# Performance work log

Hardware: AMD Instinct MI355X
Metric: run time of the kernel (lower is better)

The kernel has to match this reference:

```python
import jax, jax.numpy as jnp
import numpy as np

N = 51200      # total nodes
G = 128        # graphs
E = 614400     # edges
IN, HID, OUT = 128, 64, 64


def gcn_conv(x, W, b, src, dst, n):
    # PyG GCNConv: add self loops, symmetric normalization, aggregate src->dst
    h = x @ W                                   # [n, d_out]
    loop = jnp.arange(n)
    s = jnp.concatenate([src, loop])
    d = jnp.concatenate([dst, loop])
    deg = jax.ops.segment_sum(jnp.ones_like(d, dtype=h.dtype), d, num_segments=n)
    dinv = jnp.where(deg > 0, jax.lax.rsqrt(deg), 0.0)
    norm = dinv[s] * dinv[d]                    # [E+n]
    out = jax.ops.segment_sum(h[s] * norm[:, None], d, num_segments=n)
    return out + b


def setup_inputs() -> dict:
    key = jax.random.key(0)
    ks = jax.random.split(key, 8)
    x = jax.random.normal(ks[0], (N, IN), dtype=jnp.float32)
    edge_index = jax.random.randint(ks[1], (2, E), 0, N, dtype=jnp.int64)
    batch = jnp.repeat(jnp.arange(G, dtype=jnp.int64), N // G)   # 400 nodes/graph
    rootindex = jnp.arange(G, dtype=jnp.int64) * (N // G)
    root = jax.random.normal(ks[2], (G, IN), dtype=jnp.float32)
    W1 = jax.random.normal(ks[3], (IN, HID), dtype=jnp.float32) / np.sqrt(IN)
    b1 = jnp.zeros((HID,), dtype=jnp.float32)
    W2 = jax.random.normal(ks[4], (HID + IN, OUT), dtype=jnp.float32) / np.sqrt(HID + IN)
    b2 = jnp.zeros((OUT,), dtype=jnp.float32)
    return {"x": x, "edge_index": edge_index, "batch": batch,
            "rootindex": rootindex, "root": root,
            "W1": W1, "b1": b1, "W2": W2, "b2": b2}


def reference(x, edge_index, batch, rootindex, root, W1, b1, W2, b2):
    n = x.shape[0]
    g = root.shape[0]
    src, dst = edge_index[0], edge_index[1]

    h1 = gcn_conv(x, W1, b1, src, dst, n)        # conv1 output (= x2 in torch)
    root_extend1 = root[batch]                   # broadcast root feats to nodes
    h = jax.nn.relu(jnp.concatenate([h1, root_extend1], axis=1))
    # F.dropout(training=False) -> identity (eval mode)
    h2 = jax.nn.relu(gcn_conv(h, W2, b2, src, dst, n))
    root_extend2 = h1[rootindex][batch]          # x2[rootindex[batch_id]] per node
    out = jnp.concatenate([h2, root_extend2], axis=1)   # [N, OUT+HID]
    # scatter_mean over graphs
    counts = jax.ops.segment_sum(jnp.ones((n,), dtype=out.dtype), batch, num_segments=g)
    pooled = jax.ops.segment_sum(out, batch, num_segments=g) / counts[:, None]
    return pooled                                 # [G, OUT+HID]
```

## Files before the change

### kernel.cpp

```cpp
#include <hip/hip_runtime.h>
#include <hip/hip_bf16.h>
#include <math.h>

#define DIN 128
#define DH  64
#define CAPP 32
#define BKSH 8
#define BKN  256
#define BCAP 4096
#define BCSH 12
#define ACH  4096

typedef short  short8 __attribute__((ext_vector_type(8)));
typedef float  f32x4  __attribute__((ext_vector_type(4)));
typedef unsigned short us4 __attribute__((ext_vector_type(4)));

__device__ __forceinline__ short f2bf(float v) {
    return __builtin_bit_cast(short, __float2bfloat16(v));
}
__device__ __forceinline__ float bf2f(unsigned short v) {
    return __builtin_bit_cast(float, ((unsigned)v) << 16);
}


__device__ __forceinline__ void wpack_body(const float* __restrict__ W, short8* __restrict__ o, int fid) {
    int l  = fid & 63, f = fid >> 6;
    int kc = f >> 2, nt = f & 3;
    int kb = kc * 32 + (l >> 4) * 8;
    int c  = nt * 16 + (l & 15);
    short8 r;
    #pragma unroll
    for (int j = 0; j < 8; ++j) r[j] = f2bf(W[(size_t)(kb + j) * DH + c]);
    o[fid] = r;
}

template<int KDIM>
__device__ __forceinline__ void mgemm_body(int wid, int lane, const float* __restrict__ feat,
                                           const short8* __restrict__ wpk,
                                           unsigned short* __restrict__ out, int N) {
    constexpr int KCH = KDIM / 32;
    int ntiles = (N + 15) >> 4;
    if (wid >= ntiles) return;

    short8 bf[KCH][4];
    #pragma unroll
    for (int kc = 0; kc < KCH; ++kc)
        #pragma unroll
        for (int nt = 0; nt < 4; ++nt)
            bf[kc][nt] = wpk[(kc * 4 + nt) * 64 + lane];

    f32x4 acc[4] = {};

    int arow = wid * 16 + (lane & 15);
    if (arow >= N) arow = N - 1;

    #pragma unroll
    for (int kc = 0; kc < KCH; ++kc) {
        const float* ap = feat + (size_t)arow * KDIM + ((lane >> 4) * 8) + kc * 32;
        f32x4 a0 = *reinterpret_cast<const f32x4*>(ap);
        f32x4 a1 = *reinterpret_cast<const f32x4*>(ap + 4);
        short8 af;
        #pragma unroll
        for (int j = 0; j < 4; ++j) {
            af[j]     = f2bf(a0[j]);
            af[4 + j] = f2bf(a1[j]);
        }
        #pragma unroll
        for (int nt = 0; nt < 4; ++nt)
            acc[nt] = __builtin_amdgcn_mfma_f32_16x16x32_bf16(af, bf[kc][nt], acc[nt], 0, 0, 0);
    }

    int rbase = wid * 16 + (lane >> 4) * 4;
    int col   = lane & 15;
    #pragma unroll
    for (int q = 0; q < 4; ++q) {
        int row = rbase + q;
        if (row >= N) break;
        #pragma unroll
        for (int nt = 0; nt < 4; ++nt)
            out[(size_t)row * DH + nt * 16 + col] = (unsigned short)f2bf(acc[nt][q]);
    }
}

__device__ __forceinline__ void gsum32(const unsigned* __restrict__ row32, int cnt,
                                       const unsigned* __restrict__ feat32, int l32,
                                       float& alo, float& ahi) {
    for (int j = 0; j < cnt; ++j) {
        unsigned pa = row32[j >> 1];
        unsigned s = (j & 1) ? (pa >> 16) : (pa & 0xffffu);
        unsigned v = feat32[(size_t)s * (DH / 2) + l32];
        alo += bf2f((unsigned short)(v & 0xffffu));
        ahi += bf2f((unsigned short)(v >> 16));
    }
}

__device__ __forceinline__ void gsum_dual(const unsigned* __restrict__ rowA,
                                          const unsigned* __restrict__ rowB,
                                          int n1A, int n1B, unsigned selfA, unsigned selfB,
                                          const unsigned* __restrict__ f32p, int l32,
                                          float& aAlo, float& aAhi, float& aBlo, float& aBhi) {
    int m1 = n1A > n1B ? n1A : n1B;
    for (int j = 0; j < m1; j += 4) {
        unsigned paA = rowA[j >> 1], pbA = rowA[(j >> 1) + 1];
        unsigned paB = rowB[j >> 1], pbB = rowB[(j >> 1) + 1];
        unsigned sA0 = (j + 0 < n1A) ? (paA & 0xffffu) : selfA;
        unsigned sA1 = (j + 1 < n1A) ? (paA >> 16)     : selfA;
        unsigned sA2 = (j + 2 < n1A) ? (pbA & 0xffffu) : selfA;
        unsigned sA3 = (j + 3 < n1A) ? (pbA >> 16)     : selfA;
        unsigned sB0 = (j + 0 < n1B) ? (paB & 0xffffu) : selfB;
        unsigned sB1 = (j + 1 < n1B) ? (paB >> 16)     : selfB;
        unsigned sB2 = (j + 2 < n1B) ? (pbB & 0xffffu) : selfB;
        unsigned sB3 = (j + 3 < n1B) ? (pbB >> 16)     : selfB;
        unsigned vA0 = f32p[(size_t)sA0 * (DH / 2) + l32];
        unsigned vA1 = f32p[(size_t)sA1 * (DH / 2) + l32];
        unsigned vA2 = f32p[(size_t)sA2 * (DH / 2) + l32];
        unsigned vA3 = f32p[(size_t)sA3 * (DH / 2) + l32];
        unsigned vB0 = f32p[(size_t)sB0 * (DH / 2) + l32];
        unsigned vB1 = f32p[(size_t)sB1 * (DH / 2) + l32];
        unsigned vB2 = f32p[(size_t)sB2 * (DH / 2) + l32];
        unsigned vB3 = f32p[(size_t)sB3 * (DH / 2) + l32];
        aAlo += ((j + 0 < n1A) ? bf2f((unsigned short)(vA0 & 0xffffu)) : 0.f)
              + ((j + 1 < n1A) ? bf2f((unsigned short)(vA1 & 0xffffu)) : 0.f)
              + ((j + 2 < n1A) ? bf2f((unsigned short)(vA2 & 0xffffu)) : 0.f)
              + ((j + 3 < n1A) ? bf2f((unsigned short)(vA3 & 0xffffu)) : 0.f);
        aAhi += ((j + 0 < n1A) ? bf2f((unsigned short)(vA0 >> 16)) : 0.f)
              + ((j + 1 < n1A) ? bf2f((unsigned short)(vA1 >> 16)) : 0.f)
              + ((j + 2 < n1A) ? bf2f((unsigned short)(vA2 >> 16)) : 0.f)
              + ((j + 3 < n1A) ? bf2f((unsigned short)(vA3 >> 16)) : 0.f);
        aBlo += ((j + 0 < n1B) ? bf2f((unsigned short)(vB0 & 0xffffu)) : 0.f)
              + ((j + 1 < n1B) ? bf2f((unsigned short)(vB1 & 0xffffu)) : 0.f)
              + ((j + 2 < n1B) ? bf2f((unsigned short)(vB2 & 0xffffu)) : 0.f)
              + ((j + 3 < n1B) ? bf2f((unsigned short)(vB3 & 0xffffu)) : 0.f);
        aBhi += ((j + 0 < n1B) ? bf2f((unsigned short)(vB0 >> 16)) : 0.f)
              + ((j + 1 < n1B) ? bf2f((unsigned short)(vB1 >> 16)) : 0.f)
              + ((j + 2 < n1B) ? bf2f((unsigned short)(vB2 >> 16)) : 0.f)
              + ((j + 3 < n1B) ? bf2f((unsigned short)(vB3 >> 16)) : 0.f);
    }
}


__global__ void k_pre(const float* __restrict__ W1, const float* __restrict__ W2,
                      const float* __restrict__ root, const int* __restrict__ batch,
                      int N, int G, int NBK, int WPB, int BB,
                      short8* __restrict__ wp1, short8* __restrict__ wp2,
                      int* __restrict__ startg, int* __restrict__ endg,
                      unsigned* __restrict__ bktbase, float* __restrict__ gvv,
                      float* __restrict__ poolsum) {
    int b = blockIdx.x, tid = threadIdx.x;
    if (b < WPB) {
        int id = b * 256 + tid;
        if (id < 1024) wpack_body(W1, wp1, id);
        else if (id < 1536) wpack_body(W2, wp2, id - 1024);
    } else if (b < WPB + BB) {
        int i = (b - WPB) * 256 + tid;
        if (i >= N) return;
        if (i < NBK) bktbase[i] = 0u;
        int bb = batch[i];
        if (i == 0     || batch[i - 1] != bb) startg[bb] = i;
        if (i == N - 1 || batch[i + 1] != bb) endg[bb]   = i + 1;
    } else {
        int g    = (b - WPB - BB) * 4 + (tid >> 6);
        int lane = tid & 63;
        if (g >= G) return;
        float acc = 0.f;
        #pragma unroll
        for (int k = 0; k < DIN; ++k) {
            float r = root[g * DIN + k];
            r = r > 0.f ? r : 0.f;
            acc += r * W2[(size_t)(DH + k) * DH + lane];
        }
        gvv[g * DH + lane] = acc;
        poolsum[g * DH + lane] = 0.f;
    }
}

__global__ void k_scatgemm(const int* __restrict__ src, const int* __restrict__ dst,
                           int E, int N, int NBK, int EB,
                           unsigned* __restrict__ bktbase, unsigned* __restrict__ ebuf,
                           const float* __restrict__ x, const short8* __restrict__ wp1,
                           unsigned short* __restrict__ bufA) {
    int b = blockIdx.x, tid = threadIdx.x;
    if (b < EB) {
        __shared__ unsigned hist[BKN];
        __shared__ unsigned rbase[BKN];
        __shared__ unsigned cur[BKN];
        hist[tid] = 0;
        cur[tid] = 0;
        __syncthreads();
        int e0 = b * ACH + tid;
        #pragma unroll
        for (int k = 0; k < ACH / 256; ++k) {
            int e = e0 + k * 256;
            if (e < E) atomicAdd(&hist[dst[e] >> BKSH], 1u);
        }
        __syncthreads();
        if (tid < NBK) rbase[tid] = atomicAdd(&bktbase[tid], hist[tid]);
        __syncthreads();
        #pragma unroll
        for (int k = 0; k < ACH / 256; ++k) {
            int e = e0 + k * 256;
            if (e < E) {
                int d = dst[e];
                int bk = d >> BKSH;
                unsigned off = rbase[bk] + atomicAdd(&cur[bk], 1u);
                if (off < BCAP)
                    ebuf[((size_t)bk << BCSH) + off] =
                        ((unsigned)(d & (BKN - 1)) << 16) | (unsigned)(src[e] & 0xffff);
            }
        }
    } else {
        int wid = (b - EB) * 4 + (tid >> 6);
        mgemm_body<DIN>(wid, tid & 63, x, wp1, bufA, N);
    }
}

__global__ void k_csrscale(const unsigned* __restrict__ ebuf, const unsigned* __restrict__ blen,
                           unsigned short* __restrict__ csr32, unsigned short* __restrict__ csr2,
                           int* __restrict__ deg, unsigned short* __restrict__ bufA, int N) {
    __shared__ int cur[BKN];
    int b = blockIdx.x, tid = threadIdx.x;
    cur[tid] = 0;
    __syncthreads();
    int len = blen[b]; if (len > BCAP) len = BCAP;
    const unsigned* ep = ebuf + ((size_t)b << BCSH);
    for (int e = tid; e < len; e += 256) {
        unsigned v = ep[e];
        int d = v >> 16, s = v & 0xffff;
        int slot = atomicAdd(&cur[d], 1);
        size_t node = ((size_t)b << BKSH) + d;
        if (slot < CAPP) csr32[node * CAPP + slot] = (unsigned short)s;
        else if (slot < 2 * CAPP) csr2[node * CAPP + (slot - CAPP)] = (unsigned short)s;
    }
    __syncthreads();
    int node = (b << BKSH) + tid;
    if (node < N) deg[node] = cur[tid];

    int nodebase = b << BKSH;
    us4* rows = (us4*)bufA + (size_t)nodebase * (DH / 4);
    #pragma unroll
    for (int it = 0; it < 16; ++it) {
        int r = it * 16 + (tid >> 4);
        int c = tid & 15;
        if (nodebase + r < N) {
            float di = rsqrtf((float)(cur[r] + 1));
            us4 v = rows[(size_t)r * (DH / 4) + c];
            #pragma unroll
            for (int j = 0; j < 4; ++j) v[j] = (unsigned short)f2bf(bf2f(v[j]) * di);
            rows[(size_t)r * (DH / 4) + c] = v;
        }
    }
}

__global__ void k_conv1(const unsigned short* __restrict__ csr32, const unsigned short* __restrict__ csr2,
                        const int* __restrict__ deg, const unsigned short* __restrict__ fs1,
                        const float* __restrict__ bs1, const int* __restrict__ batch,
                        const int* __restrict__ ridx, const float* __restrict__ gv,
                        const short8* __restrict__ wp2, unsigned short* __restrict__ fs2,
                        float* __restrict__ outp, int N) {
    __shared__ unsigned short lh[16 * 72];
    __shared__ float ldi[16];
    __shared__ int   lbg[16];
    int w = threadIdx.x >> 6, lane = threadIdx.x & 63;
    int hf = lane >> 5, l32 = lane & 31;
    int base = blockIdx.x * 16;
    const unsigned* f32p = (const unsigned*)fs1;

    int nA16 = w * 4 + hf * 2, nB16 = nA16 + 1;
    int iA = base + nA16, iB = base + nB16;
    bool vA = iA < N, vB = iB < N;
    int iAc = vA ? iA : N - 1, iBc = vB ? iB : N - 1;

    int dgA = deg[iAc], dgB = deg[iBc];
    float diA = rsqrtf((float)(dgA + 1)), diB = rsqrtf((float)(dgB + 1));
    int ndA = dgA > 2 * CAPP ? 2 * CAPP : dgA, n1A = ndA > CAPP ? CAPP : ndA;
    int ndB = dgB > 2 * CAPP ? 2 * CAPP : dgB, n1B = ndB > CAPP ? CAPP : ndB;
    if (!vA) { n1A = 0; ndA = 0; }
    if (!vB) { n1B = 0; ndB = 0; }

    unsigned svA = f32p[(size_t)iAc * (DH / 2) + l32];
    unsigned svB = f32p[(size_t)iBc * (DH / 2) + l32];
    float aAlo = bf2f((unsigned short)(svA & 0xffffu)), aAhi = bf2f((unsigned short)(svA >> 16));
    float aBlo = bf2f((unsigned short)(svB & 0xffffu)), aBhi = bf2f((unsigned short)(svB >> 16));

    gsum_dual((const unsigned*)(csr32 + (size_t)iAc * CAPP),
              (const unsigned*)(csr32 + (size_t)iBc * CAPP),
              n1A, n1B, (unsigned)iAc, (unsigned)iBc, f32p, l32, aAlo, aAhi, aBlo, aBhi);
    if (ndA > CAPP) gsum32((const unsigned*)(csr2 + (size_t)iAc * CAPP), ndA - CAPP, f32p, l32, aAlo, aAhi);
    if (ndB > CAPP) gsum32((const unsigned*)(csr2 + (size_t)iBc * CAPP), ndB - CAPP, f32p, l32, aBlo, aBhi);

    float2 bv = ((const float2*)bs1)[l32];
    if (vA) {
        float h1lo = aAlo * diA + bv.x, h1hi = aAhi * diA + bv.y;
        int bg = batch[iA];
        if (ridx[bg] == iA) {
            float2 rv; rv.x = h1lo; rv.y = h1hi;
            ((float2*)(outp + (size_t)bg * (2 * DH) + DH))[l32] = rv;
        }
        unsigned packed = ((unsigned)(unsigned short)f2bf(fmaxf(h1hi, 0.f)) << 16)
                        | (unsigned short)f2bf(fmaxf(h1lo, 0.f));
        ((unsigned*)lh)[nA16 * 36 + l32] = packed;
        if (l32 == 0) { ldi[nA16] = diA; lbg[nA16] = bg; }
    }
    if (vB) {
        float h1lo = aBlo * diB + bv.x, h1hi = aBhi * diB + bv.y;
        int bg = batch[iB];
        if (ridx[bg] == iB) {
            float2 rv; rv.x = h1lo; rv.y = h1hi;
            ((float2*)(outp + (size_t)bg * (2 * DH) + DH))[l32] = rv;
        }
        unsigned packed = ((unsigned)(unsigned short)f2bf(fmaxf(h1hi, 0.f)) << 16)
                        | (unsigned short)f2bf(fmaxf(h1lo, 0.f));
        ((unsigned*)lh)[nB16 * 36 + l32] = packed;
        if (l32 == 0) { ldi[nB16] = diB; lbg[nB16] = bg; }
    }
    __syncthreads();

    short8 bq0 = wp2[(0 * 4 + w) * 64 + lane];
    short8 bq1 = wp2[(1 * 4 + w) * 64 + lane];
    const unsigned short* ap = lh + (lane & 15) * 72 + ((lane >> 4) * 8);
    short8 a0 = *reinterpret_cast<const short8*>(ap);
    short8 a1 = *reinterpret_cast<const short8*>(ap + 32);
    f32x4 acc = {};
    acc = __builtin_amdgcn_mfma_f32_16x16x32_bf16(a0, bq0, acc, 0, 0, 0);
    acc = __builtin_amdgcn_mfma_f32_16x16x32_bf16(a1, bq1, acc, 0, 0, 0);

    int lr = (lane >> 4) * 4, col = w * 16 + (lane & 15);
    #pragma unroll
    for (int q = 0; q < 4; ++q) {
        int lrow = lr + q, row = base + lrow;
        if (row >= N) break;
        float v = acc[q] + gv[lbg[lrow] * DH + col];
        v *= ldi[lrow];
        fs2[(size_t)row * DH + col] = (unsigned short)f2bf(v);
    }
}

__global__ void k_agg2pool(const unsigned short* __restrict__ csr32, const unsigned short* __restrict__ csr2,
                           const int* __restrict__ deg, const unsigned short* __restrict__ fs,
                           const float* __restrict__ b2, const int* __restrict__ batch,
                           float* __restrict__ poolsum, int N) {
    __shared__ float2 part[8][32];
    int wv = threadIdx.x >> 6, lane = threadIdx.x & 63;
    int hf = lane >> 5, l32 = lane & 31;
    int base = blockIdx.x * 16;
    int g0   = batch[base];
    const unsigned* f32p = (const unsigned*)fs;

    int iA = base + wv * 4 + hf * 2, iB = iA + 1;
    bool vA = iA < N, vB = iB < N;
    int iAc = vA ? iA : N - 1, iBc = vB ? iB : N - 1;

    int dgA = deg[iAc], dgB = deg[iBc];
    float diA = rsqrtf((float)(dgA + 1)), diB = rsqrtf((float)(dgB + 1));
    int ndA = dgA > 2 * CAPP ? 2 * CAPP : dgA, n1A = ndA > CAPP ? CAPP : ndA;
    int ndB = dgB > 2 * CAPP ? 2 * CAPP : dgB, n1B = ndB > CAPP ? CAPP : ndB;
    if (!vA) { n1A = 0; ndA = 0; }
    if (!vB) { n1B = 0; ndB = 0; }

    unsigned svA = f32p[(size_t)iAc * (DH / 2) + l32];
    unsigned svB = f32p[(size_t)iBc * (DH / 2) + l32];
    float aAlo = bf2f((unsigned short)(svA & 0xffffu)), aAhi = bf2f((unsigned short)(svA >> 16));
    float aBlo = bf2f((unsigned short)(svB & 0xffffu)), aBhi = bf2f((unsigned short)(svB >> 16));

    gsum_dual((const unsigned*)(csr32 + (size_t)iAc * CAPP),
              (const unsigned*)(csr32 + (size_t)iBc * CAPP),
              n1A, n1B, (unsigned)iAc, (unsigned)iBc, f32p, l32, aAlo, aAhi, aBlo, aBhi);
    if (ndA > CAPP) gsum32((const unsigned*)(csr2 + (size_t)iAc * CAPP), ndA - CAPP, f32p, l32, aAlo, aAhi);
    if (ndB > CAPP) gsum32((const unsigned*)(csr2 + (size_t)iBc * CAPP), ndB - CAPP, f32p, l32, aBlo, aBhi);

    float2 bv = ((const float2*)b2)[l32];
    float plo = 0.f, phi = 0.f;
    if (vA) {
        float r0 = fmaxf(aAlo * diA + bv.x, 0.f);
        float r1 = fmaxf(aAhi * diA + bv.y, 0.f);
        int bg = batch[iA];
        if (bg == g0) { plo += r0; phi += r1; }
        else {
            atomicAdd(&poolsum[bg * DH + 2 * l32],     r0);
            atomicAdd(&poolsum[bg * DH + 2 * l32 + 1], r1);
        }
    }
    if (vB) {
        float r0 = fmaxf(aBlo * diB + bv.x, 0.f);
        float r1 = fmaxf(aBhi * diB + bv.y, 0.f);
        int bg = batch[iB];
        if (bg == g0) { plo += r0; phi += r1; }
        else {
            atomicAdd(&poolsum[bg * DH + 2 * l32],     r0);
            atomicAdd(&poolsum[bg * DH + 2 * l32 + 1], r1);
        }
    }
    part[wv * 2 + hf][l32].x = plo;
    part[wv * 2 + hf][l32].y = phi;
    __syncthreads();
    if (wv == 0) {
        int fd = lane >> 1, sel = lane & 1;
        float s = 0.f;
        #pragma unroll
        for (int k = 0; k < 8; ++k) s += sel ? part[k][fd].y : part[k][fd].x;
        atomicAdd(&poolsum[g0 * DH + lane], s);
    }
}

__global__ void k_out(const float* __restrict__ poolsum, const int* __restrict__ startg,
                      const int* __restrict__ endg, float* __restrict__ outp, int G) {
    int id = blockIdx.x * blockDim.x + threadIdx.x;
    int g = id >> 6, lane = id & 63;
    if (g >= G) return;
    outp[(size_t)g * (2 * DH) + lane] = poolsum[g * DH + lane] / (float)(endg[g] - startg[g]);
}


static inline size_t align256(size_t x) { return (x + 255) & ~(size_t)255; }

extern "C" void kernel_launch(void* const* d_in, const int* in_sizes, int n_in,
                              void* d_out, int out_size, void* d_ws, size_t ws_size,
                              hipStream_t stream) {
    const float* x    = (const float*)d_in[0];
    const int*   ei   = (const int*)d_in[1];
    const int*   batch= (const int*)d_in[2];
    const int*   ridx = (const int*)d_in[3];
    const float* root = (const float*)d_in[4];
    const float* W1   = (const float*)d_in[5];
    const float* b1   = (const float*)d_in[6];
    const float* W2   = (const float*)d_in[7];
    const float* b2   = (const float*)d_in[8];
    float* out = (float*)d_out;

    const int N = in_sizes[0] / DIN;
    const int E = in_sizes[1] / 2;
    const int G = in_sizes[3];

    const int* src = ei;
    const int* dst = ei + E;

    const int NBK = N >> BKSH;
    const int EB  = (E + ACH - 1) / ACH;

    char* p = (char*)d_ws;
    int*   deg     = (int*)p;            p += align256((size_t)N * 4);
    int*   startg  = (int*)p;            p += align256((size_t)G * 4);
    int*   endg    = (int*)p;            p += align256((size_t)G * 4);
    float* gv      = (float*)p;          p += align256((size_t)G * DH * 4);
    float* poolsum = (float*)p;          p += align256((size_t)G * DH * 4);
    short8* wp1    = (short8*)p;         p += align256(1024 * sizeof(short8));
    short8* wp2    = (short8*)p;         p += align256(512  * sizeof(short8));
    unsigned* bktbase = (unsigned*)p;    p += align256((size_t)NBK * 4);
    unsigned* ebuf = (unsigned*)p;       p += align256((size_t)NBK * BCAP * 4);
    unsigned short* csr32 = (unsigned short*)p; p += align256((size_t)N * CAPP * 2);
    unsigned short* csr2  = (unsigned short*)p; p += align256((size_t)N * CAPP * 2);
    unsigned short* bufA  = (unsigned short*)p; p += align256((size_t)N * DH * 2);
    unsigned short* bufB  = (unsigned short*)p; p += align256((size_t)N * DH * 2);
    (void)ws_size; (void)n_in; (void)out_size;

    const int T  = 256;
    const int ntiles = (N + 15) / 16;
    const int WPB = 6;
    const int BB  = (N + T - 1) / T;
    const int GVB = (G + 3) / 4;
    const int GB  = (ntiles + 3) / 4;

    k_pre     <<<WPB + BB + GVB, T, 0, stream>>>(W1, W2, root, batch, N, G, NBK, WPB, BB,
                                                 wp1, wp2, startg, endg, bktbase, gv, poolsum);
    k_scatgemm<<<EB + GB, T, 0, stream>>>(src, dst, E, N, NBK, EB, bktbase, ebuf, x, wp1, bufA);
    k_csrscale<<<NBK, T, 0, stream>>>(ebuf, bktbase, csr32, csr2, deg, bufA, N);
    k_conv1   <<<ntiles, T, 0, stream>>>(csr32, csr2, deg, bufA, b1, batch, ridx,
                                         gv, wp2, bufB, out, N);
    k_agg2pool<<<(N + 15) / 16, T, 0, stream>>>(csr32, csr2, deg, bufB, b2, batch,
                                                poolsum, N);
    k_out     <<<(G * DH + T - 1) / T, T, 0, stream>>>(poolsum, startg, endg, out, G);
}
```

Baseline: 78.51 us.

## Fuse mean-pool division into aggregation kernel and widen gather unroll to eight

Drops the final k_out kernel. Each graph's output slots are zeroed in k_pre, and k_agg2pool scales its partial sums by the inverse node count before atomically adding straight into the output. Separately, the dual-row gather loop now loads eight neighbour indices per step with one 128-bit load and issues eight feature loads per row, giving more memory-level parallelism. This saves one launch and the poolsum round trip. The risks are extra divisions per atomic, possible over-reads of padded CSR rows, and a change in floating-point summation order.

```diff
diff --git a/kernel.cpp b/kernel.cpp
--- a/kernel.cpp
+++ b/kernel.cpp
@@ -100,41 +100,26 @@
                                           const unsigned* __restrict__ f32p, int l32,
                                           float& aAlo, float& aAhi, float& aBlo, float& aBhi) {
     int m1 = n1A > n1B ? n1A : n1B;
-    for (int j = 0; j < m1; j += 4) {
-        unsigned paA = rowA[j >> 1], pbA = rowA[(j >> 1) + 1];
-        unsigned paB = rowB[j >> 1], pbB = rowB[(j >> 1) + 1];
-        unsigned sA0 = (j + 0 < n1A) ? (paA & 0xffffu) : selfA;
-        unsigned sA1 = (j + 1 < n1A) ? (paA >> 16)     : selfA;
-        unsigned sA2 = (j + 2 < n1A) ? (pbA & 0xffffu) : selfA;
-        unsigned sA3 = (j + 3 < n1A) ? (pbA >> 16)     : selfA;
-        unsigned sB0 = (j + 0 < n1B) ? (paB & 0xffffu) : selfB;
-        unsigned sB1 = (j + 1 < n1B) ? (paB >> 16)     : selfB;
-        unsigned sB2 = (j + 2 < n1B) ? (pbB & 0xffffu) : selfB;
-        unsigned sB3 = (j + 3 < n1B) ? (pbB >> 16)     : selfB;
-        unsigned vA0 = f32p[(size_t)sA0 * (DH / 2) + l32];
-        unsigned vA1 = f32p[(size_t)sA1 * (DH / 2) + l32];
-        unsigned vA2 = f32p[(size_t)sA2 * (DH / 2) + l32];
-        unsigned vA3 = f32p[(size_t)sA3 * (DH / 2) + l32];
-        unsigned vB0 = f32p[(size_t)sB0 * (DH / 2) + l32];
-        unsigned vB1 = f32p[(size_t)sB1 * (DH / 2) + l32];
-        unsigned vB2 = f32p[(size_t)sB2 * (DH / 2) + l32];
-        unsigned vB3 = f32p[(size_t)sB3 * (DH / 2) + l32];
-        aAlo += ((j + 0 < n1A) ? bf2f((unsigned short)(vA0 & 0xffffu)) : 0.f)
-              + ((j + 1 < n1A) ? bf2f((unsigned short)(vA1 & 0xffffu)) : 0.f)
-              + ((j + 2 < n1A) ? bf2f((unsigned short)(vA2 & 0xffffu)) : 0.f)
-              + ((j + 3 < n1A) ? bf2f((unsigned short)(vA3 & 0xffffu)) : 0.f);
-        aAhi += ((j + 0 < n1A) ? bf2f((unsigned short)(vA0 >> 16)) : 0.f)
-              + ((j + 1 < n1A) ? bf2f((unsigned short)(vA1 >> 16)) : 0.f)
-              + ((j + 2 < n1A) ? bf2f((unsigned short)(vA2 >> 16)) : 0.f)
-              + ((j + 3 < n1A) ? bf2f((unsigned short)(vA3 >> 16)) : 0.f);
-        aBlo += ((j + 0 < n1B) ? bf2f((unsigned short)(vB0 & 0xffffu)) : 0.f)
-              + ((j + 1 < n1B) ? bf2f((unsigned short)(vB1 & 0xffffu)) : 0.f)
-              + ((j + 2 < n1B) ? bf2f((unsigned short)(vB2 & 0xffffu)) : 0.f)
-              + ((j + 3 < n1B) ? bf2f((unsigned short)(vB3 & 0xffffu)) : 0.f);
-        aBhi += ((j + 0 < n1B) ? bf2f((unsigned short)(vB0 >> 16)) : 0.f)
-              + ((j + 1 < n1B) ? bf2f((unsigned short)(vB1 >> 16)) : 0.f)
-              + ((j + 2 < n1B) ? bf2f((unsigned short)(vB2 >> 16)) : 0.f)
-              + ((j + 3 < n1B) ? bf2f((unsigned short)(vB3 >> 16)) : 0.f);
+    for (int j = 0; j < m1; j += 8) {
+        uint4 qa = *reinterpret_cast<const uint4*>(rowA + (j >> 1));
+        uint4 qb = *reinterpret_cast<const uint4*>(rowB + (j >> 1));
+        unsigned pA[4] = {qa.x, qa.y, qa.z, qa.w};
+        unsigned pB[4] = {qb.x, qb.y, qb.z, qb.w};
+        unsigned vA[8], vB[8];
+        #pragma unroll
+        for (int k = 0; k < 8; ++k) {
+            unsigned sA = (j + k < n1A) ? ((k & 1) ? (pA[k >> 1] >> 16) : (pA[k >> 1] & 0xffffu)) : selfA;
+            unsigned sB = (j + k < n1B) ? ((k & 1) ? (pB[k >> 1] >> 16) : (pB[k >> 1] & 0xffffu)) : selfB;
+            vA[k] = f32p[(size_t)sA * (DH / 2) + l32];
+            vB[k] = f32p[(size_t)sB * (DH / 2) + l32];
+        }
+        #pragma unroll
+        for (int k = 0; k < 8; ++k) {
+            aAlo += (j + k < n1A) ? bf2f((unsigned short)(vA[k] & 0xffffu)) : 0.f;
+            aAhi += (j + k < n1A) ? bf2f((unsigned short)(vA[k] >> 16))     : 0.f;
+            aBlo += (j + k < n1B) ? bf2f((unsigned short)(vB[k] & 0xffffu)) : 0.f;
+            aBhi += (j + k < n1B) ? bf2f((unsigned short)(vB[k] >> 16))     : 0.f;
+        }
     }
 }
 
@@ -145,7 +130,7 @@
                       short8* __restrict__ wp1, short8* __restrict__ wp2,
                       int* __restrict__ startg, int* __restrict__ endg,
                       unsigned* __restrict__ bktbase, float* __restrict__ gvv,
-                      float* __restrict__ poolsum) {
+                      float* __restrict__ outp) {
     int b = blockIdx.x, tid = threadIdx.x;
     if (b < WPB) {
         int id = b * 256 + tid;
@@ -170,7 +155,7 @@
             acc += r * W2[(size_t)(DH + k) * DH + lane];
         }
         gvv[g * DH + lane] = acc;
-        poolsum[g * DH + lane] = 0.f;
+        outp[(size_t)g * (2 * DH) + lane] = 0.f;
     }
 }
 
@@ -338,7 +323,8 @@
 __global__ void k_agg2pool(const unsigned short* __restrict__ csr32, const unsigned short* __restrict__ csr2,
                            const int* __restrict__ deg, const unsigned short* __restrict__ fs,
                            const float* __restrict__ b2, const int* __restrict__ batch,
-                           float* __restrict__ poolsum, int N) {
+                           const int* __restrict__ startg, const int* __restrict__ endg,
+                           float* __restrict__ outp, int N) {
     __shared__ float2 part[8][32];
     int wv = threadIdx.x >> 6, lane = threadIdx.x & 63;
     int hf = lane >> 5, l32 = lane & 31;
@@ -376,8 +362,9 @@
         int bg = batch[iA];
         if (bg == g0) { plo += r0; phi += r1; }
         else {
-            atomicAdd(&poolsum[bg * DH + 2 * l32],     r0);
-            atomicAdd(&poolsum[bg * DH + 2 * l32 + 1], r1);
+            float inv = 1.f / (float)(endg[bg] - startg[bg]);
+            atomicAdd(&outp[(size_t)bg * (2 * DH) + 2 * l32],     r0 * inv);
+            atomicAdd(&outp[(size_t)bg * (2 * DH) + 2 * l32 + 1], r1 * inv);
         }
     }
     if (vB) {
@@ -386,8 +373,9 @@
         int bg = batch[iB];
         if (bg == g0) { plo += r0; phi += r1; }
         else {
-            atomicAdd(&poolsum[bg * DH + 2 * l32],     r0);
-            atomicAdd(&poolsum[bg * DH + 2 * l32 + 1], r1);
+            float inv = 1.f / (float)(endg[bg] - startg[bg]);
+            atomicAdd(&outp[(size_t)bg * (2 * DH) + 2 * l32],     r0 * inv);
+            atomicAdd(&outp[(size_t)bg * (2 * DH) + 2 * l32 + 1], r1 * inv);
         }
     }
     part[wv * 2 + hf][l32].x = plo;
@@ -398,16 +386,9 @@
         float s = 0.f;
         #pragma unroll
         for (int k = 0; k < 8; ++k) s += sel ? part[k][fd].y : part[k][fd].x;
-        atomicAdd(&poolsum[g0 * DH + lane], s);
-    }
-}
-
-__global__ void k_out(const float* __restrict__ poolsum, const int* __restrict__ startg,
-                      const int* __restrict__ endg, float* __restrict__ outp, int G) {
-    int id = blockIdx.x * blockDim.x + threadIdx.x;
-    int g = id >> 6, lane = id & 63;
-    if (g >= G) return;
-    outp[(size_t)g * (2 * DH) + lane] = poolsum[g * DH + lane] / (float)(endg[g] - startg[g]);
+        float inv0 = 1.f / (float)(endg[g0] - startg[g0]);
+        atomicAdd(&outp[(size_t)g0 * (2 * DH) + lane], s * inv0);
+    }
 }
 
 
@@ -442,7 +423,6 @@
     int*   startg  = (int*)p;            p += align256((size_t)G * 4);
     int*   endg    = (int*)p;            p += align256((size_t)G * 4);
     float* gv      = (float*)p;          p += align256((size_t)G * DH * 4);
-    float* poolsum = (float*)p;          p += align256((size_t)G * DH * 4);
     short8* wp1    = (short8*)p;         p += align256(1024 * sizeof(short8));
     short8* wp2    = (short8*)p;         p += align256(512  * sizeof(short8));
     unsigned* bktbase = (unsigned*)p;    p += align256((size_t)NBK * 4);
@@ -461,12 +441,11 @@
     const int GB  = (ntiles + 3) / 4;
 
     k_pre     <<<WPB + BB + GVB, T, 0, stream>>>(W1, W2, root, batch, N, G, NBK, WPB, BB,
-                                                 wp1, wp2, startg, endg, bktbase, gv, poolsum);
+                                                 wp1, wp2, startg, endg, bktbase, gv, out);
     k_scatgemm<<<EB + GB, T, 0, stream>>>(src, dst, E, N, NBK, EB, bktbase, ebuf, x, wp1, bufA);
     k_csrscale<<<NBK, T, 0, stream>>>(ebuf, bktbase, csr32, csr2, deg, bufA, N);
     k_conv1   <<<ntiles, T, 0, stream>>>(csr32, csr2, deg, bufA, b1, batch, ridx,
                                          gv, wp2, bufB, out, N);
     k_agg2pool<<<(N + 15) / 16, T, 0, stream>>>(csr32, csr2, deg, bufB, b2, batch,
-                                                poolsum, N);
-    k_out     <<<(G * DH + T - 1) / T, T, 0, stream>>>(poolsum, startg, endg, out, G);
-}
+                                                startg, endg, out, N);
+}
```

New measurement: 76.31 us. -2.8%, faster.
